# Kernel tuning notes

Hardware: AMD Instinct MI355X
Metric: run time of the kernel (lower is better)

The kernel has to match this reference:

```python
import jax, jax.numpy as jnp
import numpy as np

N, E = 20000, 320000
CUR, HID, OUT, H = 256, 256, 64, 6  # cur_dim, hidden_dim, output_dim, gat heads


def setup_inputs() -> dict:
    key = jax.random.key(0)
    ks = jax.random.split(key, 16)
    p = lambda k, shape: jax.random.normal(k, shape, jnp.float32) * 0.05
    return dict(
        x=jax.random.normal(ks[0], (N, CUR), jnp.float32),
        edge_index=jax.random.randint(ks[1], (2, E), 0, N),
        edge_weight=jax.random.uniform(ks[2], (E,), jnp.float32),
        Wp=p(ks[3], (CUR, HID)), bp=p(ks[4], (HID,)),
        W_gat=p(ks[5], (HID, H * OUT)),
        att_src=p(ks[6], (H, OUT)), att_dst=p(ks[7], (H, OUT)),
        b_gat=p(ks[8], (H * OUT,)),
        W_gcn0=p(ks[9], (HID, OUT)), b_gcn0=p(ks[10], (OUT,)),
        W_gcn1=p(ks[11], (HID, OUT)), b_gcn1=p(ks[12], (OUT,)),
        W_arma_init=p(ks[13], (H * OUT, OUT)),
        W_arma_root=p(ks[14], (H * OUT, OUT)),
        b_arma=p(ks[15], (OUT,)),
    )


def _seg_sum(v, ids, n):
    return jax.ops.segment_sum(v, ids, num_segments=n)


def _gat(h, src, dst, W, a_s, a_d, b):
    # PyG GATConv: add self loops, per-edge attention, softmax over incoming edges.
    n = h.shape[0]
    loops = jnp.arange(n)
    s = jnp.concatenate([src, loops])
    d = jnp.concatenate([dst, loops])
    xw = (h @ W).reshape(n, H, OUT)               # [N,H,F]
    al = (xw * a_s).sum(-1)                       # [N,H] source term
    ar = (xw * a_d).sum(-1)                       # [N,H] target term
    e = jax.nn.leaky_relu(al[s] + ar[d], 0.2)     # [E',H]
    m = jax.ops.segment_max(e, d, num_segments=n)  # stable softmax per target
    pe = jnp.exp(e - m[d])
    alpha = pe / _seg_sum(pe, d, n)[d]
    out = _seg_sum(alpha[:, :, None] * xw[s], d, n)  # [N,H,F]
    return out.reshape(n, H * OUT) + b


def _gcn(h, src, dst, w, W, b):
    # PyG GCNConv: self loops (weight 1), symmetric D^-1/2 A D^-1/2 normalization.
    n = h.shape[0]
    loops = jnp.arange(n)
    s = jnp.concatenate([src, loops])
    d = jnp.concatenate([dst, loops])
    w2 = jnp.concatenate([w, jnp.ones((n,), h.dtype)])
    deg = _seg_sum(w2, d, n)
    dinv = jnp.where(deg > 0, jax.lax.rsqrt(deg), 0.0)
    norm = dinv[s] * w2 * dinv[d]
    xw = h @ W
    return _seg_sum(norm[:, None] * xw[s], d, n) + b


def _arma(h, src, dst, w, Wi, Wr, b):
    # PyG ARMAConv, num_stacks=1, num_layers=1, act=ReLU; gcn_norm WITHOUT self loops.
    n = h.shape[0]
    deg = _seg_sum(w, dst, n)
    dinv = jnp.where(deg > 0, jax.lax.rsqrt(deg), 0.0)
    norm = dinv[src] * w * dinv[dst]
    t = h @ Wi
    agg = _seg_sum(norm[:, None] * t[src], dst, n)
    return jax.nn.relu(agg + h @ Wr + b)


def reference(x, edge_index, edge_weight, Wp, bp, W_gat, att_src, att_dst, b_gat,
              W_gcn0, b_gcn0, W_gcn1, b_gcn1, W_arma_init, W_arma_root, b_arma):
    src, dst = edge_index[0], edge_index[1]
    h = x @ Wp + bp
    lrelu = lambda v: jax.nn.leaky_relu(v, 0.01)  # F.leaky_relu default slope
    h1 = lrelu(_gat(h, src, dst, W_gat, att_src, att_dst, b_gat))   # [N, 6*64]
    h2 = lrelu(_gcn(h, src, dst, edge_weight, W_gcn0, b_gcn0))       # [N, 64]
    h3 = lrelu(_gcn(h, src, dst, edge_weight, W_gcn1, b_gcn1))       # [N, 64]
    h4 = lrelu(_arma(h1, src, dst, edge_weight, W_arma_init, W_arma_root, b_arma))
    return jnp.tanh(jnp.concatenate([h1, h2, h3, h4], axis=1))      # [N, 576]
```

## Files before the change

### kernel.cpp

```cpp
#include <hip/hip_runtime.h>


#define NN 20000
#define EE 320000
#define GATD 384
#define NH 6
#define OUTD 64
#define ODIM 576

typedef __bf16 bf16_8 __attribute__((ext_vector_type(8)));
typedef float f32_4 __attribute__((ext_vector_type(4)));

__device__ __forceinline__ float lrelu(float x, float s) { return x > 0.f ? x : s * x; }

__device__ __forceinline__ float loadf(const void* p, size_t i, int f32) {
  return f32 ? ((const float*)p)[i] : (float)((const __bf16*)p)[i];
}

struct ProbeArgs {
  const void* ptr[15];
  int cnt[15];
  int flagidx[15];
  const int* ei;
};
__global__ void k_probe_all(ProbeArgs a, int* __restrict__ flags) {
  __shared__ int cnt;
  if (threadIdx.x == 0) cnt = 0;
  __syncthreads();
  int b = blockIdx.x;
  if (b < 15) {
    const unsigned short* u = (const unsigned short*)a.ptr[b];
    int m = a.cnt[b] < 2048 ? a.cnt[b] : 2048;
    int c = 0;
    for (int i = threadIdx.x; i < m; i += 256) {
      float v = __uint_as_float(((unsigned int)u[i]) << 16);
      if (!(fabsf(v) < 1e4f)) c++;
    }
    if (c) atomicAdd(&cnt, c);
    __syncthreads();
    if (threadIdx.x == 0) flags[a.flagidx[b]] = (cnt > m / 16) ? 1 : 0;
  } else {
    int c = 0;
    for (int i = threadIdx.x; i < 1024; i += 256)
      if (a.ei[2 * i + 1] != 0) c++;
    if (c) atomicAdd(&cnt, c);
    __syncthreads();
    if (threadIdx.x == 0) flags[16] = (cnt <= 2) ? 1 : 0;
  }
}

struct CvtSeg { const void* in; __bf16* out; int n; int flagidx; int blk0; };
struct CvtArgs { CvtSeg s[7]; };
struct TSeg { const void* in; __bf16* out; int R; int C; int flagidx; int blk0; };
struct TArgs { TSeg s[6]; };
__global__ __launch_bounds__(256) void k_cvt_count(CvtArgs ca, int ncvtblk, TArgs ta, int ncvtT,
    const int* __restrict__ flags, const int* __restrict__ ei, const void* __restrict__ ew,
    int* __restrict__ deg, float* __restrict__ wdeg) {
  int bx = blockIdx.x;
  if (bx >= ncvtT) {
    int e = (bx - ncvtT) * 256 + threadIdx.x;
    if (e >= EE) return;
    int sh = flags[16];
    int d = ei[(size_t)(EE + e) << sh];
    atomicAdd(&deg[d], 1);
    atomicAdd(&wdeg[d], loadf(ew, e, flags[2]));
    return;
  }
  if (bx < ncvtblk) {
    int b = bx;
    int k = 0;
    while (k + 1 < 7 && ca.s[k + 1].blk0 <= b) k++;
    const CvtSeg sg = ca.s[k];
    int i = (b - sg.blk0) * 256 + threadIdx.x;
    if (i >= sg.n) return;
    sg.out[i] = flags[sg.flagidx] ? (__bf16)((const float*)sg.in)[i] : ((const __bf16*)sg.in)[i];
    return;
  }
  __shared__ float t[32][33];
  int b = bx - ncvtblk;
  int k = 0;
  while (k + 1 < 6 && ta.s[k + 1].blk0 <= b) k++;
  const TSeg sg = ta.s[k];
  int f32 = flags[sg.flagidx];
  int tpx = (sg.C + 31) >> 5;
  int lt = b - sg.blk0;
  int c0 = (lt % tpx) * 32, r0 = (lt / tpx) * 32;
  int tid = threadIdx.x;
  for (int idx = tid; idx < 1024; idx += 256) {
    int r = idx >> 5, c = idx & 31;
    if (r0 + r < sg.R && c0 + c < sg.C)
      t[r][c] = loadf(sg.in, (size_t)(r0 + r) * sg.C + (c0 + c), f32);
  }
  __syncthreads();
  for (int idx = tid; idx < 1024; idx += 256) {
    int r = idx >> 5, c = idx & 31;
    if (c0 + r < sg.C && r0 + c < sg.R)
      sg.out[(size_t)(c0 + r) * sg.R + (r0 + c)] = (__bf16)t[c][r];
  }
}

__global__ __launch_bounds__(256) void k_scan1(const int* __restrict__ deg,
                                               int* __restrict__ bsum) {
  int i = blockIdx.x * 256 + threadIdx.x;
  int v = (i < NN) ? deg[i] : 0;
  for (int off = 32; off; off >>= 1) v += __shfl_xor(v, off);
  __shared__ int ws[4];
  if ((threadIdx.x & 63) == 0) ws[threadIdx.x >> 6] = v;
  __syncthreads();
  if (threadIdx.x == 0) bsum[blockIdx.x] = ws[0] + ws[1] + ws[2] + ws[3];
}

__device__ __forceinline__ void scan2_body(int b, const int* __restrict__ deg,
    const int* __restrict__ bsum, const float* __restrict__ wdeg,
    int* __restrict__ rowstart, float* __restrict__ dg, float* __restrict__ da) {
  int tid = threadIdx.x;
  int lane = tid & 63, wv = tid >> 6;
  int i = b * 256 + tid;
  __shared__ int red[4];
  __shared__ int wsum2[4];
  __shared__ int sbase;
  {
    int v = (tid < b) ? bsum[tid] : 0;
    for (int off = 32; off; off >>= 1) v += __shfl_xor(v, off);
    if (lane == 0) red[wv] = v;
    __syncthreads();
    if (tid == 0) sbase = red[0] + red[1] + red[2] + red[3];
    __syncthreads();
  }
  int v = (i < NN) ? deg[i] : 0;
  int run = v;
  for (int off = 1; off < 64; off <<= 1) {
    int u = __shfl_up(run, off);
    if (lane >= off) run += u;
  }
  if (lane == 63) wsum2[wv] = run;
  __syncthreads();
  int wb = 0;
#pragma unroll
  for (int w = 0; w < 4; w++) { int x = wsum2[w]; if (w < wv) wb += x; }
  int excl = sbase + wb + run - v;
  if (i < NN) rowstart[i] = excl;
  if (i == NN - 1) rowstart[NN] = excl + v;
  if (i < NN) {
    float w = wdeg[i];
    dg[i] = rsqrtf(w + 1.0f);
    da[i] = w > 0.f ? rsqrtf(w) : 0.f;
  }
}

__device__ __forceinline__ void fill_body(int b, const int* __restrict__ ei,
    const void* __restrict__ ew, const int* __restrict__ flags,
    const int* __restrict__ rowstart, int* __restrict__ cursor,
    int* __restrict__ csr_src, float* __restrict__ csr_w) {
  int e = b * 256 + threadIdx.x;
  if (e >= EE) return;
  int sh = flags[16];
  int d = ei[(size_t)(EE + e) << sh];
  int s = ei[(size_t)e << sh];
  int pos = rowstart[d] + atomicAdd(&cursor[d], 1);
  csr_src[pos] = s;
  csr_w[pos] = loadf(ew, e, flags[2]);
}

__device__ __forceinline__ void gemm_body(const void* __restrict__ A,
    const int* __restrict__ aflag, const __bf16* __restrict__ Bt,
    const __bf16* __restrict__ bias,
    __bf16* __restrict__ C1, int n1, int ldc1,
    __bf16* __restrict__ C2, int ldc2,
    int M, int K, int bx, int by) {
  __shared__ __bf16 Al[64][40];
  __shared__ __bf16 Bl[128][40];
  int a32 = *aflag;
  int tid = threadIdx.x;
  int w = tid >> 6, lane = tid & 63;
  int quad = lane >> 4, r = lane & 15;
  int row0 = bx * 64, col0 = by * 128;
  f32_4 acc[4][2] = {};
  int srow = tid >> 2;
  int koff = (tid & 3) * 8;
  int brow = tid >> 1;
  int bko  = (tid & 1) * 16;
  for (int kt = 0; kt < K; kt += 32) {
    int arow = row0 + srow;
    if (a32) {
      float4 a0 = {0.f, 0.f, 0.f, 0.f}, a1 = {0.f, 0.f, 0.f, 0.f};
      if (arow < M) {
        const float* ap = (const float*)A + (size_t)arow * K + kt + koff;
        a0 = *(const float4*)ap;
        a1 = *(const float4*)(ap + 4);
      }
      bf16_8 t;
      t[0] = (__bf16)a0.x; t[1] = (__bf16)a0.y; t[2] = (__bf16)a0.z; t[3] = (__bf16)a0.w;
      t[4] = (__bf16)a1.x; t[5] = (__bf16)a1.y; t[6] = (__bf16)a1.z; t[7] = (__bf16)a1.w;
      *(bf16_8*)(&Al[srow][koff]) = t;
    } else {
      float4 av = {0.f, 0.f, 0.f, 0.f};
      if (arow < M) av = *(const float4*)((const __bf16*)A + (size_t)arow * K + kt + koff);
      *(float4*)(&Al[srow][koff]) = av;
    }
    const __bf16* bp = Bt + (size_t)(col0 + brow) * K + kt + bko;
    *(float4*)(&Bl[brow][bko])     = *(const float4*)bp;
    *(float4*)(&Bl[brow][bko + 8]) = *(const float4*)(bp + 8);
    __syncthreads();
    bf16_8 bfrag0 = *(const bf16_8*)(&Bl[w * 16 + r][quad * 8]);
    bf16_8 bfrag1 = *(const bf16_8*)(&Bl[64 + w * 16 + r][quad * 8]);
#pragma unroll
    for (int mt = 0; mt < 4; mt++) {
      bf16_8 afrag = *(const bf16_8*)(&Al[mt * 16 + r][quad * 8]);
      acc[mt][0] = __builtin_amdgcn_mfma_f32_16x16x32_bf16(afrag, bfrag0, acc[mt][0], 0, 0, 0);
      acc[mt][1] = __builtin_amdgcn_mfma_f32_16x16x32_bf16(afrag, bfrag1, acc[mt][1], 0, 0, 0);
    }
    __syncthreads();
  }
  __bf16* Cp; int ldc; int cbase;
  if (col0 < n1) { Cp = C1; ldc = ldc1; cbase = col0; }
  else           { Cp = C2; ldc = ldc2; cbase = col0 - n1; }
  int cc0 = cbase + w * 16 + r;
  int cc1 = cbase + 64 + w * 16 + r;
  float bv0 = bias ? (float)bias[col0 + w * 16 + r] : 0.0f;
  float bv1 = bias ? (float)bias[col0 + 64 + w * 16 + r] : 0.0f;
#pragma unroll
  for (int mt = 0; mt < 4; mt++) {
#pragma unroll
    for (int rr = 0; rr < 4; rr++) {
      int crow = row0 + mt * 16 + quad * 4 + rr;
      if (crow < M) {
        Cp[(size_t)crow * ldc + cc0] = (__bf16)(acc[mt][0][rr] + bv0);
        Cp[(size_t)crow * ldc + cc1] = (__bf16)(acc[mt][1][rr] + bv1);
      }
    }
  }
}

__global__ __launch_bounds__(256) void k_gemm(const void* __restrict__ A,
    const int* __restrict__ aflag, const __bf16* __restrict__ Bt,
    const __bf16* __restrict__ bias,
    __bf16* __restrict__ C1, int n1, int ldc1,
    __bf16* __restrict__ C2, int ldc2, int M, int K) {
  gemm_body(A, aflag, Bt, bias, C1, n1, ldc1, C2, ldc2, M, K, blockIdx.x, blockIdx.y);
}

__global__ __launch_bounds__(256) void k_gemm1_scan2(const void* __restrict__ A,
    const int* __restrict__ aflag, const __bf16* __restrict__ Bt,
    const __bf16* __restrict__ bias, __bf16* __restrict__ C1, int M, int K, int ngemm,
    const int* __restrict__ deg, const int* __restrict__ bsum,
    const float* __restrict__ wdeg, int* __restrict__ rowstart,
    float* __restrict__ dg, float* __restrict__ da) {
  int bx = blockIdx.x;
  if (bx < ngemm) {
    gemm_body(A, aflag, Bt, bias, C1, 256, 256, nullptr, 0, M, K, bx % 313, bx / 313);
  } else {
    scan2_body(bx - ngemm, deg, bsum, wdeg, rowstart, dg, da);
  }
}

__global__ __launch_bounds__(256) void k_gemm2_fill(const void* __restrict__ A,
    const int* __restrict__ aflag, const __bf16* __restrict__ Bt,
    __bf16* __restrict__ C1, int n1, int ldc1, __bf16* __restrict__ C2, int ldc2,
    int M, int K, int ngemm,
    const int* __restrict__ ei, const void* __restrict__ ew,
    const int* __restrict__ flags, const int* __restrict__ rowstart,
    int* __restrict__ cursor, int* __restrict__ csr_src, float* __restrict__ csr_w) {
  int bx = blockIdx.x;
  if (bx < ngemm) {
    gemm_body(A, aflag, Bt, nullptr, C1, n1, ldc1, C2, ldc2, M, K, bx % 313, bx / 313);
  } else {
    fill_body(bx - ngemm, ei, ew, flags, rowstart, cursor, csr_src, csr_w);
  }
}

__global__ void k_alar_w(const __bf16* __restrict__ xwb, const __bf16* __restrict__ as_,
                         const __bf16* __restrict__ ad_,
                         float* __restrict__ al, float* __restrict__ ar) {
  int p = blockIdx.x * 4 + (threadIdx.x >> 6);
  int lane = threadIdx.x & 63;
  if (p >= NN * NH) return;
  int i = p / NH, h = p - i * NH;
  float xv = (float)xwb[(size_t)i * GATD + h * OUTD + lane];
  float s1 = xv * (float)as_[h * OUTD + lane];
  float s2 = xv * (float)ad_[h * OUTD + lane];
  for (int off = 32; off; off >>= 1) { s1 += __shfl_xor(s1, off); s2 += __shfl_xor(s2, off); }
  if (lane == 0) { al[p] = s1; ar[p] = s2; }
}

__global__ __launch_bounds__(256) void k_gatgcn(const __bf16* __restrict__ xwb,
    const __bf16* __restrict__ xwgb,
    const float* __restrict__ al, const float* __restrict__ ar,
    const int* __restrict__ rowstart, const int* __restrict__ csr_src,
    const float* __restrict__ csr_w, const float* __restrict__ dgcn,
    const __bf16* __restrict__ bgat, const __bf16* __restrict__ b0,
    const __bf16* __restrict__ b1,
    __bf16* __restrict__ h1b, float* __restrict__ out) {
  int wv = threadIdx.x >> 6, lane = threadIdx.x & 63;
  int i = blockIdx.x * 4 + wv;
  __shared__ int   src_sh[4][64];
  __shared__ float ex_sh[4][64][NH];
  __shared__ float wg_sh[4][64];
  __shared__ int   mc_sh[4];
  int e0 = rowstart[i], e1 = rowstart[i + 1];
  if (lane == 0) mc_sh[wv] = (e1 - e0 + 63) >> 6;
  float arv[NH], exs[NH], acc[NH], denp[NH];
#pragma unroll
  for (int h = 0; h < NH; h++) arv[h] = ar[i * NH + h];
#pragma unroll
  for (int h = 0; h < NH; h++) {
    float e = lrelu(al[i * NH + h] + arv[h], 0.2f);
    exs[h] = __expf(e);
    acc[h] = exs[h] * (float)xwb[(size_t)i * GATD + h * OUTD + lane];
    denp[h] = 0.f;
  }
  float g0 = 0.f, g1 = 0.f;
  __syncthreads();
  int mch = max(max(mc_sh[0], mc_sh[1]), max(mc_sh[2], mc_sh[3]));
  for (int c = 0; c < mch; c++) {
    if (c) __syncthreads();
    int base = e0 + c * 64;
    int cnt = e1 - base; cnt = cnt < 0 ? 0 : (cnt > 64 ? 64 : cnt);
    if (lane < cnt) {
      int eidx = base + lane;
      int s = csr_src[eidx];
      src_sh[wv][lane] = s;
      wg_sh[wv][lane] = dgcn[s] * csr_w[eidx];
#pragma unroll
      for (int h = 0; h < NH; h++) {
        float ex = __expf(lrelu(al[s * NH + h] + arv[h], 0.2f));
        ex_sh[wv][lane][h] = ex;
        denp[h] += ex;
      }
    }
    __syncthreads();
    int j = 0;
    for (; j + 2 <= cnt; j += 2) {
      int s0 = src_sh[wv][j], s1 = src_sh[wv][j + 1];
      const __bf16* r0 = xwb + (size_t)s0 * GATD + lane;
      const __bf16* r1 = xwb + (size_t)s1 * GATD + lane;
      const __bf16* p0 = xwgb + (size_t)s0 * 128;
      const __bf16* p1 = xwgb + (size_t)s1 * 128;
      float x0[NH], x1[NH];
#pragma unroll
      for (int h = 0; h < NH; h++) { x0[h] = (float)r0[h * OUTD]; x1[h] = (float)r1[h * OUTD]; }
      float y00 = (float)p0[lane], y01 = (float)p0[lane + 64];
      float y10 = (float)p1[lane], y11 = (float)p1[lane + 64];
      float wg0 = wg_sh[wv][j], wg1 = wg_sh[wv][j + 1];
#pragma unroll
      for (int h = 0; h < NH; h++)
        acc[h] += ex_sh[wv][j][h] * x0[h] + ex_sh[wv][j + 1][h] * x1[h];
      g0 += wg0 * y00 + wg1 * y10;
      g1 += wg0 * y01 + wg1 * y11;
    }
    if (j < cnt) {
      int s0 = src_sh[wv][j];
      const __bf16* r0 = xwb + (size_t)s0 * GATD + lane;
      const __bf16* p0 = xwgb + (size_t)s0 * 128;
      float wg0 = wg_sh[wv][j];
#pragma unroll
      for (int h = 0; h < NH; h++) acc[h] += ex_sh[wv][j][h] * (float)r0[h * OUTD];
      g0 += wg0 * (float)p0[lane];
      g1 += wg0 * (float)p0[lane + 64];
    }
  }
#pragma unroll
  for (int h = 0; h < NH; h++) {
    float d = denp[h];
    for (int off = 32; off; off >>= 1) d += __shfl_xor(d, off);
    d += exs[h];
    float v = acc[h] / d + (float)bgat[h * OUTD + lane];
    v = lrelu(v, 0.01f);
    h1b[(size_t)i * GATD + h * OUTD + lane] = (__bf16)v;
    out[(size_t)i * ODIM + h * OUTD + lane] = tanhf(v);
  }
  float di = dgcn[i];
  float v0 = lrelu(di * g0 + di * di * (float)xwgb[(size_t)i * 128 + lane] + (float)b0[lane], 0.01f);
  float v1 = lrelu(di * g1 + di * di * (float)xwgb[(size_t)i * 128 + 64 + lane] + (float)b1[lane], 0.01f);
  out[(size_t)i * ODIM + 384 + lane] = tanhf(v0);
  out[(size_t)i * ODIM + 448 + lane] = tanhf(v1);
}

__global__ __launch_bounds__(256) void k_arma(const __bf16* __restrict__ trb,
    const int* __restrict__ rowstart, const int* __restrict__ csr_src,
    const float* __restrict__ csr_w, const float* __restrict__ darma,
    const __bf16* __restrict__ ba, float* __restrict__ out) {
  int wv = threadIdx.x >> 6, lane = threadIdx.x & 63;
  int i = blockIdx.x * 4 + wv;
  __shared__ __attribute__((aligned(16))) int   src_sh[4][64];
  __shared__ __attribute__((aligned(16))) float wa_sh[4][64];
  __shared__ int mc_sh[4];
  int e0 = rowstart[i], e1 = rowstart[i + 1];
  if (lane == 0) mc_sh[wv] = (e1 - e0 + 63) >> 6;
  __syncthreads();
  int mch = max(max(mc_sh[0], mc_sh[1]), max(mc_sh[2], mc_sh[3]));
  float aa = 0.f;
  for (int c = 0; c < mch; c++) {
    if (c) __syncthreads();
    int base = e0 + c * 64;
    int cnt = e1 - base; cnt = cnt < 0 ? 0 : (cnt > 64 ? 64 : cnt);
    int s = i; float wav = 0.f;
    if (lane < cnt) {
      int eidx = base + lane;
      s = csr_src[eidx];
      wav = darma[s] * csr_w[eidx];
    }
    src_sh[wv][lane] = s;
    wa_sh[wv][lane] = wav;
    __syncthreads();
    int cntp = (cnt + 7) & ~7;
    for (int j = 0; j < cntp; j += 8) {
      int4 sa = *(const int4*)&src_sh[wv][j];
      int4 sb = *(const int4*)&src_sh[wv][j + 4];
      int sq[8] = {sa.x, sa.y, sa.z, sa.w, sb.x, sb.y, sb.z, sb.w};
      float tq[8];
#pragma unroll
      for (int q = 0; q < 8; q++)
        tq[q] = (float)trb[(size_t)sq[q] * 128 + lane];
      float4 wa0 = *(const float4*)&wa_sh[wv][j];
      float4 wa1 = *(const float4*)&wa_sh[wv][j + 4];
      float waq[8] = {wa0.x, wa0.y, wa0.z, wa0.w, wa1.x, wa1.y, wa1.z, wa1.w};
#pragma unroll
      for (int q = 0; q < 8; q++) aa += waq[q] * tq[q];
    }
  }
  float va = darma[i] * aa + (float)trb[(size_t)i * 128 + 64 + lane] + (float)ba[lane];
  va = fmaxf(va, 0.f);
  out[(size_t)i * ODIM + 512 + lane] = tanhf(va);
}

extern "C" void kernel_launch(void* const* d_in, const int* in_sizes, int n_in,
                              void* d_out, int out_size, void* d_ws, size_t ws_size,
                              hipStream_t stream) {
  const int* ei = (const int*)d_in[1];
  float* out = (float*)d_out;

  char* ws = (char*)d_ws;
  size_t off = 0;
  auto alloc = [&](size_t bytes) -> void* {
    void* p = ws + off;
    off += (bytes + 255) & ~(size_t)255;
    return p;
  };
  int*    flags    = (int*)alloc(32 * 4);
  int*    deg      = (int*)alloc((size_t)3 * NN * 4);
  int*    cursor   = deg + NN;
  float*  wdeg     = (float*)(deg + 2 * NN);
  int*    bsum     = (int*)alloc(128 * 4);
  int*    rowstart = (int*)alloc((size_t)(NN + 1) * 4);
  int*    csr_src  = (int*)alloc((size_t)EE * 4);
  float*  csr_w    = (float*)alloc((size_t)EE * 4);
  float*  dgcn     = (float*)alloc((size_t)NN * 4);
  float*  darma    = (float*)alloc((size_t)NN * 4);
  float*  al       = (float*)alloc((size_t)NN * NH * 4);
  float*  ar       = (float*)alloc((size_t)NN * NH * 4);
  __bf16* bpb   = (__bf16*)alloc(256 * 2);
  __bf16* asb   = (__bf16*)alloc(384 * 2);
  __bf16* adb   = (__bf16*)alloc(384 * 2);
  __bf16* bgatb = (__bf16*)alloc(384 * 2);
  __bf16* bg0b  = (__bf16*)alloc(64 * 2);
  __bf16* bg1b  = (__bf16*)alloc(64 * 2);
  __bf16* bab   = (__bf16*)alloc(64 * 2);
  __bf16* Wp_t    = (__bf16*)alloc(256 * 256 * 2);
  __bf16* Wcat_t  = (__bf16*)alloc((size_t)(384 + 128) * 256 * 2);
  __bf16* Wgat_t  = Wcat_t;
  __bf16* Wg01_t  = Wcat_t + (size_t)384 * 256;
  __bf16* Warma_t = (__bf16*)alloc(128 * 384 * 2);
  char* regA = (char*)alloc((size_t)NN * GATD * 2);
  __bf16* h   = (__bf16*)regA;
  __bf16* h1b = (__bf16*)regA;
  char* regB = (char*)alloc((size_t)NN * GATD * 2);
  __bf16* xwb = (__bf16*)regB;
  __bf16* trb = (__bf16*)regB;
  __bf16* xwgb = (__bf16*)alloc((size_t)NN * 128 * 2);
  (void)ws_size; (void)in_sizes; (void)n_in; (void)out_size;

  hipMemsetAsync(ws, 0, 256 + (size_t)3 * NN * 4, stream);

  dim3 tb(256);
  ProbeArgs pa;
  const int pidx[15] = {0, 2, 3, 4, 5, 6, 7, 8, 9, 10, 11, 12, 13, 14, 15};
  const int pcnt[15] = {NN * 256, EE, 256 * 256, 256, 256 * 384, NH * OUTD, NH * OUTD,
                        NH * OUTD, 256 * 64, 64, 256 * 64, 64, GATD * OUTD, GATD * OUTD, 64};
  for (int k = 0; k < 15; k++) { pa.ptr[k] = d_in[pidx[k]]; pa.cnt[k] = pcnt[k]; pa.flagidx[k] = pidx[k]; }
  pa.ei = ei;
  k_probe_all<<<dim3(16), tb, 0, stream>>>(pa, flags);

  CvtArgs ca;
  TArgs ta;
  int cvtblk = 0, tblk = 0;
  {
    struct { int idx; __bf16* out; int n; } cv[7] = {
      {4, bpb, 256}, {6, asb, 384}, {7, adb, 384}, {8, bgatb, 384},
      {10, bg0b, 64}, {12, bg1b, 64}, {15, bab, 64},
    };
    for (int k = 0; k < 7; k++) {
      ca.s[k].in = d_in[cv[k].idx]; ca.s[k].out = cv[k].out; ca.s[k].n = cv[k].n;
      ca.s[k].flagidx = cv[k].idx; ca.s[k].blk0 = cvtblk;
      cvtblk += (cv[k].n + 255) / 256;
    }
    struct { int idx; __bf16* out; int R; int C; } tv[6] = {
      {3,  Wp_t,             256, 256},
      {5,  Wgat_t,           256, 384},
      {9,  Wg01_t,           256, 64},
      {11, Wg01_t + 64 * 256, 256, 64},
      {13, Warma_t,          384, 64},
      {14, Warma_t + 64 * 384, 384, 64},
    };
    for (int k = 0; k < 6; k++) {
      ta.s[k].in = d_in[tv[k].idx]; ta.s[k].out = tv[k].out;
      ta.s[k].R = tv[k].R; ta.s[k].C = tv[k].C;
      ta.s[k].flagidx = tv[k].idx; ta.s[k].blk0 = tblk;
      tblk += ((tv[k].R + 31) / 32) * ((tv[k].C + 31) / 32);
    }
  }
  const int EEBLK = (EE + 255) / 256;
  const int NBLK  = (NN + 255) / 256;
  const int MB64  = (NN + 63) / 64;
  int ncvtT = cvtblk + tblk;
  k_cvt_count<<<dim3(ncvtT + EEBLK), tb, 0, stream>>>(ca, cvtblk, ta, ncvtT,
                                                      flags, ei, d_in[2], deg, wdeg);

  k_scan1<<<dim3(NBLK), tb, 0, stream>>>(deg, bsum);

  k_gemm1_scan2<<<dim3(313 * 2 + NBLK), tb, 0, stream>>>(d_in[0], &flags[0], Wp_t, bpb,
      h, NN, 256, 313 * 2, deg, bsum, wdeg, rowstart, dgcn, darma);

  k_gemm2_fill<<<dim3(313 * 4 + EEBLK), tb, 0, stream>>>(h, &flags[30], Wcat_t,
      xwb, 384, 384, xwgb, 128, NN, 256, 313 * 4,
      ei, d_in[2], flags, rowstart, cursor, csr_src, csr_w);

  k_alar_w<<<dim3((NN * NH + 3) / 4), tb, 0, stream>>>(xwb, asb, adb, al, ar);
  k_gatgcn<<<dim3(NN / 4), tb, 0, stream>>>(xwb, xwgb, al, ar, rowstart, csr_src,
                                            csr_w, dgcn, bgatb, bg0b, bg1b, h1b, out);
  k_gemm<<<dim3(MB64, 1), tb, 0, stream>>>(h1b, &flags[30], Warma_t, nullptr,
                                           trb, 128, 128, nullptr, 0, NN, 384);
  k_arma<<<dim3(NN / 4), tb, 0, stream>>>(trb, rowstart, csr_src, csr_w,
                                          darma, bab, out);
}
```

Measured before the change: 285.3 us.

## Split GAT/GCN node edges across two wavefronts and fold memset into probe

```diff
diff --git a/kernel.cpp b/kernel.cpp
--- a/kernel.cpp
+++ b/kernel.cpp
@@ -23,11 +23,16 @@
   int flagidx[15];
   const int* ei;
 };
-__global__ void k_probe_all(ProbeArgs a, int* __restrict__ flags) {
+__global__ void k_probe_all(ProbeArgs a, int* __restrict__ flags, int* __restrict__ zbase) {
+  int b = blockIdx.x;
+  if (b >= 16) {
+    int idx = (b - 16) * 256 + threadIdx.x;
+    if (idx < (3 * NN) / 4) ((int4*)zbase)[idx] = make_int4(0, 0, 0, 0);
+    return;
+  }
   __shared__ int cnt;
   if (threadIdx.x == 0) cnt = 0;
   __syncthreads();
-  int b = blockIdx.x;
   if (b < 15) {
     const unsigned short* u = (const unsigned short*)a.ptr[b];
     int m = a.cnt[b] < 2048 ? a.cnt[b] : 2048;
@@ -45,7 +50,7 @@
       if (a.ei[2 * i + 1] != 0) c++;
     if (c) atomicAdd(&cnt, c);
     __syncthreads();
-    if (threadIdx.x == 0) flags[16] = (cnt <= 2) ? 1 : 0;
+    if (threadIdx.x == 0) { flags[16] = (cnt <= 2) ? 1 : 0; flags[30] = 0; }
   }
 }
 
@@ -288,92 +293,121 @@
     const float* __restrict__ al, const float* __restrict__ ar,
     const int* __restrict__ rowstart, const int* __restrict__ csr_src,
     const float* __restrict__ csr_w, const float* __restrict__ dgcn,
-    const __bf16* __restrict__ bgat, const __bf16* __restrict__ b0,
-    const __bf16* __restrict__ b1,
+    const __bf16* __restrict__ bgat, const __bf16* __restrict__ b0v,
+    const __bf16* __restrict__ b1v,
     __bf16* __restrict__ h1b, float* __restrict__ out) {
-  int wv = threadIdx.x >> 6, lane = threadIdx.x & 63;
-  int i = blockIdx.x * 4 + wv;
+  int tid = threadIdx.x;
+  int wv = tid >> 6, lane = tid & 63;
+  int nd = wv >> 1, half = wv & 1;
+  int i = blockIdx.x * 2 + nd;
   __shared__ int   src_sh[4][64];
   __shared__ float ex_sh[4][64][NH];
   __shared__ float wg_sh[4][64];
+  __shared__ float comb_sh[2][8][64];
+  __shared__ float denp_sh[2][2][NH];
   __shared__ int   mc_sh[4];
   int e0 = rowstart[i], e1 = rowstart[i + 1];
-  if (lane == 0) mc_sh[wv] = (e1 - e0 + 63) >> 6;
+  int deg = e1 - e0;
+  int em = e0 + ((deg + 1) >> 1);
+  int rb0 = half ? em : e0;
+  int rb1 = half ? e1 : em;
+  if (lane == 0) mc_sh[wv] = (rb1 - rb0 + 63) >> 6;
   float arv[NH], exs[NH], acc[NH], denp[NH];
 #pragma unroll
   for (int h = 0; h < NH; h++) arv[h] = ar[i * NH + h];
 #pragma unroll
-  for (int h = 0; h < NH; h++) {
-    float e = lrelu(al[i * NH + h] + arv[h], 0.2f);
-    exs[h] = __expf(e);
-    acc[h] = exs[h] * (float)xwb[(size_t)i * GATD + h * OUTD + lane];
-    denp[h] = 0.f;
+  for (int h = 0; h < NH; h++) { acc[h] = 0.f; denp[h] = 0.f; exs[h] = 0.f; }
+  if (half == 0) {
+#pragma unroll
+    for (int h = 0; h < NH; h++) {
+      float e = lrelu(al[i * NH + h] + arv[h], 0.2f);
+      exs[h] = __expf(e);
+      acc[h] = exs[h] * (float)xwb[(size_t)i * GATD + h * OUTD + lane];
+    }
   }
   float g0 = 0.f, g1 = 0.f;
   __syncthreads();
   int mch = max(max(mc_sh[0], mc_sh[1]), max(mc_sh[2], mc_sh[3]));
   for (int c = 0; c < mch; c++) {
     if (c) __syncthreads();
-    int base = e0 + c * 64;
-    int cnt = e1 - base; cnt = cnt < 0 ? 0 : (cnt > 64 ? 64 : cnt);
+    int base = rb0 + c * 64;
+    int cnt = rb1 - base; cnt = cnt < 0 ? 0 : (cnt > 64 ? 64 : cnt);
+    int s = i; float wg = 0.f;
+    float exh[NH];
+#pragma unroll
+    for (int h = 0; h < NH; h++) exh[h] = 0.f;
     if (lane < cnt) {
       int eidx = base + lane;
-      int s = csr_src[eidx];
-      src_sh[wv][lane] = s;
-      wg_sh[wv][lane] = dgcn[s] * csr_w[eidx];
-#pragma unroll
-      for (int h = 0; h < NH; h++) {
-        float ex = __expf(lrelu(al[s * NH + h] + arv[h], 0.2f));
-        ex_sh[wv][lane][h] = ex;
-        denp[h] += ex;
+      s = csr_src[eidx];
+      float wvv = csr_w[eidx];
+      wg = dgcn[s] * wvv;
+#pragma unroll
+      for (int h = 0; h < NH; h++)
+        exh[h] = __expf(lrelu(al[s * NH + h] + arv[h], 0.2f));
+    }
+    src_sh[wv][lane] = s;
+    wg_sh[wv][lane] = wg;
+#pragma unroll
+    for (int h = 0; h < NH; h++) { ex_sh[wv][lane][h] = exh[h]; denp[h] += exh[h]; }
+    __syncthreads();
+    int cntp = (cnt + 3) & ~3;
+    for (int j = 0; j < cntp; j += 4) {
+      int4 ss = *(const int4*)&src_sh[wv][j];
+      int sq[4] = {ss.x, ss.y, ss.z, ss.w};
+      float x[4][NH], y[4][2];
+#pragma unroll
+      for (int q = 0; q < 4; q++) {
+        const __bf16* rq = xwb + (size_t)sq[q] * GATD + lane;
+#pragma unroll
+        for (int h = 0; h < NH; h++) x[q][h] = (float)rq[h * OUTD];
       }
-    }
-    __syncthreads();
-    int j = 0;
-    for (; j + 2 <= cnt; j += 2) {
-      int s0 = src_sh[wv][j], s1 = src_sh[wv][j + 1];
-      const __bf16* r0 = xwb + (size_t)s0 * GATD + lane;
-      const __bf16* r1 = xwb + (size_t)s1 * GATD + lane;
-      const __bf16* p0 = xwgb + (size_t)s0 * 128;
-      const __bf16* p1 = xwgb + (size_t)s1 * 128;
-      float x0[NH], x1[NH];
-#pragma unroll
-      for (int h = 0; h < NH; h++) { x0[h] = (float)r0[h * OUTD]; x1[h] = (float)r1[h * OUTD]; }
-      float y00 = (float)p0[lane], y01 = (float)p0[lane + 64];
-      float y10 = (float)p1[lane], y11 = (float)p1[lane + 64];
-      float wg0 = wg_sh[wv][j], wg1 = wg_sh[wv][j + 1];
-#pragma unroll
-      for (int h = 0; h < NH; h++)
-        acc[h] += ex_sh[wv][j][h] * x0[h] + ex_sh[wv][j + 1][h] * x1[h];
-      g0 += wg0 * y00 + wg1 * y10;
-      g1 += wg0 * y01 + wg1 * y11;
-    }
-    if (j < cnt) {
-      int s0 = src_sh[wv][j];
-      const __bf16* r0 = xwb + (size_t)s0 * GATD + lane;
-      const __bf16* p0 = xwgb + (size_t)s0 * 128;
-      float wg0 = wg_sh[wv][j];
-#pragma unroll
-      for (int h = 0; h < NH; h++) acc[h] += ex_sh[wv][j][h] * (float)r0[h * OUTD];
-      g0 += wg0 * (float)p0[lane];
-      g1 += wg0 * (float)p0[lane + 64];
-    }
+#pragma unroll
+      for (int q = 0; q < 4; q++) {
+        const __bf16* pq = xwgb + (size_t)sq[q] * 128;
+        y[q][0] = (float)pq[lane];
+        y[q][1] = (float)pq[lane + 64];
+      }
+#pragma unroll
+      for (int q = 0; q < 4; q++) {
+        const float* ep = ex_sh[wv][j + q];
+        float wgq = wg_sh[wv][j + q];
+#pragma unroll
+        for (int h = 0; h < NH; h++) acc[h] += ep[h] * x[q][h];
+        g0 += wgq * y[q][0];
+        g1 += wgq * y[q][1];
+      }
+    }
+  }
+  if (half == 1) {
+#pragma unroll
+    for (int h = 0; h < NH; h++) comb_sh[nd][h][lane] = acc[h];
+    comb_sh[nd][6][lane] = g0;
+    comb_sh[nd][7][lane] = g1;
   }
 #pragma unroll
   for (int h = 0; h < NH; h++) {
     float d = denp[h];
     for (int off = 32; off; off >>= 1) d += __shfl_xor(d, off);
-    d += exs[h];
-    float v = acc[h] / d + (float)bgat[h * OUTD + lane];
-    v = lrelu(v, 0.01f);
-    h1b[(size_t)i * GATD + h * OUTD + lane] = (__bf16)v;
-    out[(size_t)i * ODIM + h * OUTD + lane] = tanhf(v);
-  }
-  float di = dgcn[i];
-  float v0 = lrelu(di * g0 + di * di * (float)xwgb[(size_t)i * 128 + lane] + (float)b0[lane], 0.01f);
-  float v1 = lrelu(di * g1 + di * di * (float)xwgb[(size_t)i * 128 + 64 + lane] + (float)b1[lane], 0.01f);
-  out[(size_t)i * ODIM + 384 + lane] = tanhf(v0);
-  out[(size_t)i * ODIM + 448 + lane] = tanhf(v1);
+    if (lane == 0) denp_sh[nd][half][h] = d;
+  }
+  __syncthreads();
+  if (half == 0) {
+#pragma unroll
+    for (int h = 0; h < NH; h++) {
+      float d = denp_sh[nd][0][h] + denp_sh[nd][1][h] + exs[h];
+      float v = (acc[h] + comb_sh[nd][h][lane]) / d + (float)bgat[h * OUTD + lane];
+      v = lrelu(v, 0.01f);
+      h1b[(size_t)i * GATD + h * OUTD + lane] = (__bf16)v;
+      out[(size_t)i * ODIM + h * OUTD + lane] = tanhf(v);
+    }
+    g0 += comb_sh[nd][6][lane];
+    g1 += comb_sh[nd][7][lane];
+    float di = dgcn[i];
+    float v0 = lrelu(di * g0 + di * di * (float)xwgb[(size_t)i * 128 + lane] + (float)b0v[lane], 0.01f);
+    float v1 = lrelu(di * g1 + di * di * (float)xwgb[(size_t)i * 128 + 64 + lane] + (float)b1v[lane], 0.01f);
+    out[(size_t)i * ODIM + 384 + lane] = tanhf(v0);
+    out[(size_t)i * ODIM + 448 + lane] = tanhf(v1);
+  }
 }
 
 __global__ __launch_bounds__(256) void k_arma(const __bf16* __restrict__ trb,
@@ -470,8 +504,6 @@
   __bf16* xwgb = (__bf16*)alloc((size_t)NN * 128 * 2);
   (void)ws_size; (void)in_sizes; (void)n_in; (void)out_size;
 
-  hipMemsetAsync(ws, 0, 256 + (size_t)3 * NN * 4, stream);
-
   dim3 tb(256);
   ProbeArgs pa;
   const int pidx[15] = {0, 2, 3, 4, 5, 6, 7, 8, 9, 10, 11, 12, 13, 14, 15};
@@ -479,7 +511,8 @@
                         NH * OUTD, 256 * 64, 64, 256 * 64, 64, GATD * OUTD, GATD * OUTD, 64};
   for (int k = 0; k < 15; k++) { pa.ptr[k] = d_in[pidx[k]]; pa.cnt[k] = pcnt[k]; pa.flagidx[k] = pidx[k]; }
   pa.ei = ei;
-  k_probe_all<<<dim3(16), tb, 0, stream>>>(pa, flags);
+  const int ZBLK = ((3 * NN) / 4 + 255) / 256;
+  k_probe_all<<<dim3(16 + ZBLK), tb, 0, stream>>>(pa, flags, deg);
 
   CvtArgs ca;
   TArgs ta;
@@ -526,7 +559,7 @@
       ei, d_in[2], flags, rowstart, cursor, csr_src, csr_w);
 
   k_alar_w<<<dim3((NN * NH + 3) / 4), tb, 0, stream>>>(xwb, asb, adb, al, ar);
-  k_gatgcn<<<dim3(NN / 4), tb, 0, stream>>>(xwb, xwgb, al, ar, rowstart, csr_src,
+  k_gatgcn<<<dim3(NN / 2), tb, 0, stream>>>(xwb, xwgb, al, ar, rowstart, csr_src,
                                             csr_w, dgcn, bgatb, bg0b, bg1b, h1b, out);
   k_gemm<<<dim3(MB64, 1), tb, 0, stream>>>(h1b, &flags[30], Warma_t, nullptr,
                                            trb, 128, 128, nullptr, 0, NN, 384);
```

Result: slower. 305.5 us (+7.1%).

## Fold GAT attention vectors into weights and fuse al/ar into gemm2 launch

Applied to the files above, without the earlier changes.

```diff
diff --git a/kernel.cpp b/kernel.cpp
--- a/kernel.cpp
+++ b/kernel.cpp
@@ -23,11 +23,16 @@
   int flagidx[15];
   const int* ei;
 };
-__global__ void k_probe_all(ProbeArgs a, int* __restrict__ flags) {
+__global__ void k_probe_all(ProbeArgs a, int* __restrict__ flags, int* __restrict__ zbase) {
+  int b = blockIdx.x;
+  if (b >= 16) {
+    int idx = (b - 16) * 256 + threadIdx.x;
+    if (idx < (3 * NN) / 4) ((int4*)zbase)[idx] = make_int4(0, 0, 0, 0);
+    return;
+  }
   __shared__ int cnt;
   if (threadIdx.x == 0) cnt = 0;
   __syncthreads();
-  int b = blockIdx.x;
   if (b < 15) {
     const unsigned short* u = (const unsigned short*)a.ptr[b];
     int m = a.cnt[b] < 2048 ? a.cnt[b] : 2048;
@@ -45,7 +50,7 @@
       if (a.ei[2 * i + 1] != 0) c++;
     if (c) atomicAdd(&cnt, c);
     __syncthreads();
-    if (threadIdx.x == 0) flags[16] = (cnt <= 2) ? 1 : 0;
+    if (threadIdx.x == 0) { flags[16] = (cnt <= 2) ? 1 : 0; flags[30] = 0; }
   }
 }
 
@@ -99,15 +104,33 @@
   }
 }
 
+#define NBLK_SCAN 79
 __global__ __launch_bounds__(256) void k_scan1(const int* __restrict__ deg,
-                                               int* __restrict__ bsum) {
-  int i = blockIdx.x * 256 + threadIdx.x;
+    int* __restrict__ bsum, const __bf16* __restrict__ Wgat_t,
+    const __bf16* __restrict__ asb, const __bf16* __restrict__ adb,
+    float* __restrict__ wad) {
+  int b = blockIdx.x;
+  if (b >= NBLK_SCAN) {
+    int t = threadIdx.x;
+#pragma unroll
+    for (int jj = 0; jj < 4; jj++) {
+      int j = (b - NBLK_SCAN) * 4 + jj;
+      int h2 = j < 6 ? j : j - 6;
+      const __bf16* vec = j < 6 ? asb : adb;
+      float s = 0.f;
+      for (int f = 0; f < 64; f++)
+        s += (float)Wgat_t[(size_t)(h2 * 64 + f) * 256 + t] * (float)vec[h2 * 64 + f];
+      wad[j * 256 + t] = s;
+    }
+    return;
+  }
+  int i = b * 256 + threadIdx.x;
   int v = (i < NN) ? deg[i] : 0;
   for (int off = 32; off; off >>= 1) v += __shfl_xor(v, off);
   __shared__ int ws[4];
   if ((threadIdx.x & 63) == 0) ws[threadIdx.x >> 6] = v;
   __syncthreads();
-  if (threadIdx.x == 0) bsum[blockIdx.x] = ws[0] + ws[1] + ws[2] + ws[3];
+  if (threadIdx.x == 0) bsum[b] = ws[0] + ws[1] + ws[2] + ws[3];
 }
 
 __device__ __forceinline__ void scan2_body(int b, const int* __restrict__ deg,
@@ -162,14 +185,15 @@
   csr_w[pos] = loadf(ew, e, flags[2]);
 }
 
+#define GEMM_LDS 15360
 __device__ __forceinline__ void gemm_body(const void* __restrict__ A,
     const int* __restrict__ aflag, const __bf16* __restrict__ Bt,
     const __bf16* __restrict__ bias,
     __bf16* __restrict__ C1, int n1, int ldc1,
     __bf16* __restrict__ C2, int ldc2,
-    int M, int K, int bx, int by) {
-  __shared__ __bf16 Al[64][40];
-  __shared__ __bf16 Bl[128][40];
+    int M, int K, int bx, int by, char* pool) {
+  __bf16 (*Al)[40] = (__bf16(*)[40])pool;
+  __bf16 (*Bl)[40] = (__bf16(*)[40])(pool + 64 * 40 * 2);
   int a32 = *aflag;
   int tid = threadIdx.x;
   int w = tid >> 6, lane = tid & 63;
@@ -237,7 +261,8 @@
     const __bf16* __restrict__ bias,
     __bf16* __restrict__ C1, int n1, int ldc1,
     __bf16* __restrict__ C2, int ldc2, int M, int K) {
-  gemm_body(A, aflag, Bt, bias, C1, n1, ldc1, C2, ldc2, M, K, blockIdx.x, blockIdx.y);
+  __shared__ __attribute__((aligned(16))) char pool[GEMM_LDS];
+  gemm_body(A, aflag, Bt, bias, C1, n1, ldc1, C2, ldc2, M, K, blockIdx.x, blockIdx.y, pool);
 }
 
 __global__ __launch_bounds__(256) void k_gemm1_scan2(const void* __restrict__ A,
@@ -246,9 +271,10 @@
     const int* __restrict__ deg, const int* __restrict__ bsum,
     const float* __restrict__ wdeg, int* __restrict__ rowstart,
     float* __restrict__ dg, float* __restrict__ da) {
+  __shared__ __attribute__((aligned(16))) char pool[GEMM_LDS];
   int bx = blockIdx.x;
   if (bx < ngemm) {
-    gemm_body(A, aflag, Bt, bias, C1, 256, 256, nullptr, 0, M, K, bx % 313, bx / 313);
+    gemm_body(A, aflag, Bt, bias, C1, 256, 256, nullptr, 0, M, K, bx % 313, bx / 313, pool);
   } else {
     scan2_body(bx - ngemm, deg, bsum, wdeg, rowstart, dg, da);
   }
@@ -257,30 +283,53 @@
 __global__ __launch_bounds__(256) void k_gemm2_fill(const void* __restrict__ A,
     const int* __restrict__ aflag, const __bf16* __restrict__ Bt,
     __bf16* __restrict__ C1, int n1, int ldc1, __bf16* __restrict__ C2, int ldc2,
-    int M, int K, int ngemm,
+    int M, int K, int ngemm, int nfill,
     const int* __restrict__ ei, const void* __restrict__ ew,
     const int* __restrict__ flags, const int* __restrict__ rowstart,
-    int* __restrict__ cursor, int* __restrict__ csr_src, float* __restrict__ csr_w) {
+    int* __restrict__ cursor, int* __restrict__ csr_src, float* __restrict__ csr_w,
+    const float* __restrict__ wad, float* __restrict__ al, float* __restrict__ ar) {
+  __shared__ __attribute__((aligned(16))) char pool[GEMM_LDS];
   int bx = blockIdx.x;
   if (bx < ngemm) {
-    gemm_body(A, aflag, Bt, nullptr, C1, n1, ldc1, C2, ldc2, M, K, bx % 313, bx / 313);
-  } else {
+    gemm_body(A, aflag, Bt, nullptr, C1, n1, ldc1, C2, ldc2, M, K, bx % 313, bx / 313, pool);
+    return;
+  }
+  if (bx < ngemm + nfill) {
     fill_body(bx - ngemm, ei, ew, flags, rowstart, cursor, csr_src, csr_w);
-  }
-}
-
-__global__ void k_alar_w(const __bf16* __restrict__ xwb, const __bf16* __restrict__ as_,
-                         const __bf16* __restrict__ ad_,
-                         float* __restrict__ al, float* __restrict__ ar) {
-  int p = blockIdx.x * 4 + (threadIdx.x >> 6);
-  int lane = threadIdx.x & 63;
-  if (p >= NN * NH) return;
-  int i = p / NH, h = p - i * NH;
-  float xv = (float)xwb[(size_t)i * GATD + h * OUTD + lane];
-  float s1 = xv * (float)as_[h * OUTD + lane];
-  float s2 = xv * (float)ad_[h * OUTD + lane];
-  for (int off = 32; off; off >>= 1) { s1 += __shfl_xor(s1, off); s2 += __shfl_xor(s2, off); }
-  if (lane == 0) { al[p] = s1; ar[p] = s2; }
+    return;
+  }
+  int b2 = bx - ngemm - nfill;
+  float* wadL = (float*)pool;
+  int t = threadIdx.x;
+  for (int idx = t; idx < 12 * 256; idx += 256) wadL[idx] = wad[idx];
+  __syncthreads();
+  int i = b2 * 64 + (t >> 2);
+  int q = t & 3;
+  float p[12];
+#pragma unroll
+  for (int j = 0; j < 12; j++) p[j] = 0.f;
+  if (i < NN) {
+    const __bf16* hp = (const __bf16*)A + (size_t)i * 256 + q * 64;
+    for (int kk = 0; kk < 8; kk++) {
+      bf16_8 hv = *(const bf16_8*)(hp + kk * 8);
+#pragma unroll
+      for (int e = 0; e < 8; e++) {
+        float hf = (float)hv[e];
+        int k = q * 64 + kk * 8 + e;
+#pragma unroll
+        for (int j = 0; j < 12; j++) p[j] += hf * wadL[j * 256 + k];
+      }
+    }
+  }
+#pragma unroll
+  for (int j = 0; j < 12; j++) {
+    p[j] += __shfl_down(p[j], 1);
+    p[j] += __shfl_down(p[j], 2);
+  }
+  if (q == 0 && i < NN) {
+#pragma unroll
+    for (int h2 = 0; h2 < 6; h2++) { al[i * 6 + h2] = p[h2]; ar[i * 6 + h2] = p[6 + h2]; }
+  }
 }
 
 __global__ __launch_bounds__(256) void k_gatgcn(const __bf16* __restrict__ xwb,
@@ -442,6 +491,7 @@
   int*    cursor   = deg + NN;
   float*  wdeg     = (float*)(deg + 2 * NN);
   int*    bsum     = (int*)alloc(128 * 4);
+  float*  wad      = (float*)alloc(12 * 256 * 4);
   int*    rowstart = (int*)alloc((size_t)(NN + 1) * 4);
   int*    csr_src  = (int*)alloc((size_t)EE * 4);
   float*  csr_w    = (float*)alloc((size_t)EE * 4);
@@ -470,8 +520,6 @@
   __bf16* xwgb = (__bf16*)alloc((size_t)NN * 128 * 2);
   (void)ws_size; (void)in_sizes; (void)n_in; (void)out_size;
 
-  hipMemsetAsync(ws, 0, 256 + (size_t)3 * NN * 4, stream);
-
   dim3 tb(256);
   ProbeArgs pa;
   const int pidx[15] = {0, 2, 3, 4, 5, 6, 7, 8, 9, 10, 11, 12, 13, 14, 15};
@@ -479,7 +527,8 @@
                         NH * OUTD, 256 * 64, 64, 256 * 64, 64, GATD * OUTD, GATD * OUTD, 64};
   for (int k = 0; k < 15; k++) { pa.ptr[k] = d_in[pidx[k]]; pa.cnt[k] = pcnt[k]; pa.flagidx[k] = pidx[k]; }
   pa.ei = ei;
-  k_probe_all<<<dim3(16), tb, 0, stream>>>(pa, flags);
+  const int ZBLK = ((3 * NN) / 4 + 255) / 256;
+  k_probe_all<<<dim3(16 + ZBLK), tb, 0, stream>>>(pa, flags, deg);
 
   CvtArgs ca;
   TArgs ta;
@@ -510,22 +559,20 @@
     }
   }
   const int EEBLK = (EE + 255) / 256;
-  const int NBLK  = (NN + 255) / 256;
   const int MB64  = (NN + 63) / 64;
   int ncvtT = cvtblk + tblk;
   k_cvt_count<<<dim3(ncvtT + EEBLK), tb, 0, stream>>>(ca, cvtblk, ta, ncvtT,
                                                       flags, ei, d_in[2], deg, wdeg);
 
-  k_scan1<<<dim3(NBLK), tb, 0, stream>>>(deg, bsum);
-
-  k_gemm1_scan2<<<dim3(313 * 2 + NBLK), tb, 0, stream>>>(d_in[0], &flags[0], Wp_t, bpb,
+  k_scan1<<<dim3(NBLK_SCAN + 3), tb, 0, stream>>>(deg, bsum, Wgat_t, asb, adb, wad);
+
+  k_gemm1_scan2<<<dim3(313 * 2 + NBLK_SCAN), tb, 0, stream>>>(d_in[0], &flags[0], Wp_t, bpb,
       h, NN, 256, 313 * 2, deg, bsum, wdeg, rowstart, dgcn, darma);
 
-  k_gemm2_fill<<<dim3(313 * 4 + EEBLK), tb, 0, stream>>>(h, &flags[30], Wcat_t,
-      xwb, 384, 384, xwgb, 128, NN, 256, 313 * 4,
-      ei, d_in[2], flags, rowstart, cursor, csr_src, csr_w);
-
-  k_alar_w<<<dim3((NN * NH + 3) / 4), tb, 0, stream>>>(xwb, asb, adb, al, ar);
+  k_gemm2_fill<<<dim3(313 * 4 + EEBLK + MB64), tb, 0, stream>>>(h, &flags[30], Wcat_t,
+      xwb, 384, 384, xwgb, 128, NN, 256, 313 * 4, EEBLK,
+      ei, d_in[2], flags, rowstart, cursor, csr_src, csr_w, wad, al, ar);
+
   k_gatgcn<<<dim3(NN / 4), tb, 0, stream>>>(xwb, xwgb, al, ar, rowstart, csr_src,
                                             csr_w, dgcn, bgatb, bg0b, bg1b, h1b, out);
   k_gemm<<<dim3(MB64, 1), tb, 0, stream>>>(h1b, &flags[30], Warma_t, nullptr,
```

Result: slower. 291.6 us (+2.2%).
